# Performance work log

Hardware: AMD Instinct MI355X
Metric: run time of the kernel (lower is better)

## Reference

```python
import math
import jax, jax.numpy as jnp
import numpy as np

B, T, D = 2, 2048, 2048
H = 16
HD = D // H  # 128


def setup_inputs() -> dict:
    key = jax.random.key(0)
    k1, k2, k3 = jax.random.split(key, 3)
    x = jax.random.normal(k1, (B, T, D), dtype=jnp.float32)
    # Linear weights stored as [in, out] for x @ W (torch Linear weight is [out,in])
    w_attn = jax.random.normal(k2, (D, 3 * D), dtype=jnp.float32) * (1.0 / math.sqrt(D))
    w_proj = jax.random.normal(k3, (D, D), dtype=jnp.float32) * (1.0 / math.sqrt(D))
    return {"x": x, "w_attn": w_attn, "w_proj": w_proj}


def reference(x, w_attn, w_proj):
    Bc, Tc, Dc = x.shape
    qkv = x @ w_attn  # [B, T, 3D]
    q, k, v = jnp.split(qkv, 3, axis=2)
    # [B, H, T, HD]
    q = q.reshape(Bc, Tc, H, HD).transpose(0, 2, 1, 3)
    k = k.reshape(Bc, Tc, H, HD).transpose(0, 2, 1, 3)
    v = v.reshape(Bc, Tc, H, HD).transpose(0, 2, 1, 3)
    att = jnp.einsum('bhqd,bhkd->bhqk', q, k) * (1.0 / math.sqrt(HD))
    causal = jnp.tril(jnp.ones((Tc, Tc), dtype=bool))
    att = jnp.where(causal[None, None], att, -jnp.inf)
    att = jax.nn.softmax(att, axis=-1)
    y = jnp.einsum('bhqk,bhkd->bhqd', att, v)
    y = y.transpose(0, 2, 1, 3).reshape(Bc, Tc, Dc)
    return y @ w_proj
```

## Files before the change

kernel.cpp:

```cpp
#include <hip/hip_runtime.h>
#include <hip/hip_bf16.h>

#define B_ 2
#define T_ 2048
#define D_ 2048
#define H_ 16
#define HD_ 128
#define N3_ (3 * D_)
#define M_ (B_ * T_)

typedef __attribute__((ext_vector_type(8))) short short8;
typedef __attribute__((ext_vector_type(4))) short short4v;
typedef __attribute__((ext_vector_type(4))) float floatx4;

__device__ __forceinline__ ushort f2bf(float f) {
  unsigned int x = __float_as_uint(f);
  unsigned int r = (x + 0x7fffu + ((x >> 16) & 1u)) >> 16;
  return (ushort)r;
}

__device__ __forceinline__ void gload_lds16(const ushort* g, ushort* l) {
  __builtin_amdgcn_global_load_lds(
      (const __attribute__((address_space(1))) void*)g,
      (__attribute__((address_space(3))) void*)l, 16, 0, 0);
}

#define CONVB 4096
#define WATB 12288
#define WPTB 4096
__global__ __launch_bounds__(256) void prep(const float* __restrict__ x,
                                            const float* __restrict__ wa,
                                            const float* __restrict__ wp,
                                            ushort* __restrict__ xb,
                                            ushort* __restrict__ wt_attn,
                                            ushort* __restrict__ wt_proj) {
  __shared__ ushort tile[32][33];
  int bid = blockIdx.x;
  if (bid < CONVB) {
    int i = bid * 2048 + threadIdx.x * 8;
    union { ushort u[8]; short8 v; } t;
#pragma unroll
    for (int j = 0; j < 8; j++) t.u[j] = f2bf(x[i + j]);
    *(short8*)(xb + i) = t.v;
    return;
  }
  const float* in;
  ushort* out;
  int N, bx, by;
  if (bid < CONVB + WATB) {
    int id = bid - CONVB;
    N = N3_; bx = id % 192; by = id / 192; in = wa; out = wt_attn;
  } else {
    int id = bid - (CONVB + WATB);
    N = D_; bx = id & 63; by = id >> 6; in = wp; out = wt_proj;
  }
  int n0 = bx * 32, k0 = by * 32;
  int tx = threadIdx.x & 31, ty = threadIdx.x >> 5;
#pragma unroll
  for (int i = ty; i < 32; i += 8)
    tile[i][tx] = f2bf(in[(size_t)(k0 + i) * N + n0 + tx]);
  __syncthreads();
#pragma unroll
  for (int i = ty; i < 32; i += 8)
    out[(size_t)(n0 + i) * 2048 + k0 + tx] = tile[tx][i];
}

__device__ __forceinline__ void gemm128_core(const ushort* __restrict__ Ab,
                                             const ushort* __restrict__ Bb,
                                             ushort* As, ushort* Bs,
                                             floatx4 (&acc)[4][4]) {
  const int K = 2048;
  int tid = threadIdx.x, lane = tid & 63, wave = tid >> 6;
  int l16 = lane & 15, quad = lane >> 4;
  int srow = wave * 16 + (lane >> 2);
  int skq = (lane & 3) * 8;
  const ushort* ag = Ab + (size_t)srow * K + skq;
  const ushort* bg = Bb + (size_t)srow * K + skq;
  ushort* asl = As + wave * 512;
  ushort* bsl = Bs + wave * 512;
  int wr = wave >> 1, wc = wave & 1;
  const int aoff = (wr * 64 + l16) * 32 + quad * 8;
  const int boff = (wc * 64 + l16) * 32 + quad * 8;

  for (int k0 = 0; k0 < K; k0 += 32) {
    __syncthreads();
    gload_lds16(ag + k0, asl);
    gload_lds16(ag + (size_t)64 * K + k0, asl + 2048);
    gload_lds16(bg + k0, bsl);
    gload_lds16(bg + (size_t)64 * K + k0, bsl + 2048);
    __syncthreads();
    short8 af[4], bf[4];
#pragma unroll
    for (int mi = 0; mi < 4; mi++)
      af[mi] = *(const short8*)(As + aoff + mi * 512);
#pragma unroll
    for (int nj = 0; nj < 4; nj++)
      bf[nj] = *(const short8*)(Bs + boff + nj * 512);
#pragma unroll
    for (int mi = 0; mi < 4; mi++)
#pragma unroll
      for (int nj = 0; nj < 4; nj++)
        acc[mi][nj] = __builtin_amdgcn_mfma_f32_16x16x32_bf16(
            af[mi], bf[nj], acc[mi][nj], 0, 0, 0);
  }
}

__global__ __launch_bounds__(256) void gemm_qkv(const ushort* __restrict__ X,
                                                const ushort* __restrict__ Wt,
                                                ushort* __restrict__ qb,
                                                ushort* __restrict__ kb,
                                                ushort* __restrict__ vst) {
  __shared__ ushort As[4096], Bs[4096];
  floatx4 acc[4][4];
#pragma unroll
  for (int i = 0; i < 4; i++)
#pragma unroll
    for (int j = 0; j < 4; j++) acc[i][j] = (floatx4){0.f, 0.f, 0.f, 0.f};

  int m0 = blockIdx.y * 128, n0 = blockIdx.x * 128;
  gemm128_core(X + (size_t)m0 * 2048, Wt + (size_t)n0 * 2048, As, Bs, acc);

  int lane = threadIdx.x & 63, wave = threadIdx.x >> 6;
  int l16 = lane & 15, quad = lane >> 4, wr = wave >> 1, wc = wave & 1;
  int region = n0 >> 11;
  int h = (n0 & 2047) >> 7;
  int b = m0 >> 11, tb = m0 & 2047;
  if (region == 0) {
    ushort* P = qb + ((size_t)(b * H_ + h) * T_ + tb) * HD_;
#pragma unroll
    for (int mi = 0; mi < 4; mi++)
#pragma unroll
      for (int nj = 0; nj < 4; nj++)
#pragma unroll
        for (int r = 0; r < 4; r++)
          P[(size_t)(wr * 64 + mi * 16 + quad * 4 + r) * HD_ + wc * 64 +
            nj * 16 + l16] = f2bf(acc[mi][nj][r]);
  } else if (region == 1) {
    ushort* base = kb + (size_t)(b * H_ + h) * T_ * HD_;
#pragma unroll
    for (int mi = 0; mi < 4; mi++)
#pragma unroll
      for (int nj = 0; nj < 4; nj++) {
        int d = wc * 64 + nj * 16 + l16;
        int dhi = d >> 5, dlo = d & 31;
#pragma unroll
        for (int r = 0; r < 4; r++) {
          int t = tb + wr * 64 + mi * 16 + quad * 4 + r;
          base[(size_t)(t >> 6) * 8192 + dhi * 2048 + (t & 63) * 32 + dlo] =
              f2bf(acc[mi][nj][r]);
        }
      }
  } else {
    ushort* base = vst + (size_t)(b * H_ + h) * T_ * HD_;
#pragma unroll
    for (int mi = 0; mi < 4; mi++)
#pragma unroll
      for (int r = 0; r < 4; r++) {
        int t = tb + wr * 64 + mi * 16 + quad * 4 + r;
        int c = t & 63;
        int p = (c & 15) * 4 + (c >> 4);
        size_t rowbase = (size_t)(t >> 6) * 8192 + (p >> 5) * 4096 + (p & 31);
#pragma unroll
        for (int nj = 0; nj < 4; nj++) {
          int d = wc * 64 + nj * 16 + l16;
          base[rowbase + d * 32] = f2bf(acc[mi][nj][r]);
        }
      }
  }
}

__global__ __launch_bounds__(256) void gemm_proj(const ushort* __restrict__ Y,
                                                 const ushort* __restrict__ Wt,
                                                 float* __restrict__ out) {
  __shared__ ushort As[4096], Bs[4096];
  floatx4 acc[4][4];
#pragma unroll
  for (int i = 0; i < 4; i++)
#pragma unroll
    for (int j = 0; j < 4; j++) acc[i][j] = (floatx4){0.f, 0.f, 0.f, 0.f};

  int m0 = blockIdx.y * 128, n0 = blockIdx.x * 128;
  gemm128_core(Y + (size_t)m0 * 2048, Wt + (size_t)n0 * 2048, As, Bs, acc);

  int lane = threadIdx.x & 63, wave = threadIdx.x >> 6;
  int l16 = lane & 15, quad = lane >> 4, wr = wave >> 1, wc = wave & 1;
#pragma unroll
  for (int mi = 0; mi < 4; mi++)
#pragma unroll
    for (int nj = 0; nj < 4; nj++)
#pragma unroll
      for (int r = 0; r < 4; r++)
        out[(size_t)(m0 + wr * 64 + mi * 16 + quad * 4 + r) * D_ + n0 +
            wc * 64 + nj * 16 + l16] = acc[mi][nj][r];
}

__global__ __launch_bounds__(256) void attn128(const ushort* __restrict__ qb,
                                               const ushort* __restrict__ kst,
                                               const ushort* __restrict__ vst,
                                               ushort* __restrict__ y) {
  __shared__ ushort Ks[8192];
  __shared__ ushort Vs[8192];
  __shared__ ushort Ps[8192];
  int bid = blockIdx.x;
  int bh = bid & 31;
  int qt = (bid < 256) ? (bid >> 5) : (15 - ((bid - 256) >> 5));
  int q0 = qt * 128;
  int tid = threadIdx.x, lane = tid & 63, wave = tid >> 6;
  int l16 = lane & 15, quad = lane >> 4;
  int b = bh >> 4, h = bh & 15;
  const ushort* Q = qb + (size_t)bh * T_ * HD_;
  const ushort* Kt = kst + (size_t)bh * T_ * HD_;
  const ushort* Vt = vst + (size_t)bh * T_ * HD_;
  int qw0 = q0 + wave * 32;

  short8 qf[2][4];
#pragma unroll
  for (int mi = 0; mi < 2; mi++)
#pragma unroll
    for (int kk = 0; kk < 4; kk++)
      qf[mi][kk] = *(const short8*)(Q + (size_t)(qw0 + mi * 16 + l16) * HD_ +
                                    kk * 32 + quad * 8);

  floatx4 o[2][8];
#pragma unroll
  for (int mi = 0; mi < 2; mi++)
#pragma unroll
    for (int nt = 0; nt < 8; nt++) o[mi][nt] = (floatx4){0.f, 0.f, 0.f, 0.f};
  float lrow[2][4];
#pragma unroll
  for (int mi = 0; mi < 2; mi++)
#pragma unroll
    for (int r = 0; r < 4; r++) lrow[mi][r] = 0.f;

  const float scale2 = 0.08838834764831845f * 1.4426950408889634f;
  int ktiles = (q0 >> 6) + 2;

  for (int tile = 0; tile < ktiles; tile++) {
    int kt = tile << 6;
    __syncthreads();
#pragma unroll
    for (int i = 0; i < 4; i++) {
      int g = i * 256 + wave * 64;
      gload_lds16(Kt + (size_t)tile * 8192 + (g + lane) * 8, Ks + g * 8);
      gload_lds16(Vt + (size_t)tile * 8192 + (g + lane) * 8, Vs + g * 8);
    }
    __syncthreads();
    if (kt <= qw0 + 31) {
      floatx4 s[2][4];
#pragma unroll
      for (int mi = 0; mi < 2; mi++)
#pragma unroll
        for (int ng = 0; ng < 4; ng++) s[mi][ng] = (floatx4){0.f, 0.f, 0.f, 0.f};
#pragma unroll
      for (int kk = 0; kk < 4; kk++) {
        short8 kf[4];
#pragma unroll
        for (int ng = 0; ng < 4; ng++)
          kf[ng] = *(const short8*)(Ks + kk * 2048 + (ng * 16 + l16) * 32 +
                                    quad * 8);
#pragma unroll
        for (int mi = 0; mi < 2; mi++)
#pragma unroll
          for (int ng = 0; ng < 4; ng++)
            s[mi][ng] = __builtin_amdgcn_mfma_f32_16x16x32_bf16(
                qf[mi][kk], kf[ng], s[mi][ng], 0, 0, 0);
      }
      if (kt + 63 > qw0) {
#pragma unroll
        for (int mi = 0; mi < 2; mi++)
#pragma unroll
          for (int ng = 0; ng < 4; ng++)
#pragma unroll
            for (int r = 0; r < 4; r++) {
              int key = kt + ng * 16 + l16;
              int qr = qw0 + mi * 16 + quad * 4 + r;
              float p =
                  (key <= qr) ? exp2f(s[mi][ng][r] * scale2) : 0.f;
              s[mi][ng][r] = p;
              lrow[mi][r] += p;
            }
      } else {
#pragma unroll
        for (int mi = 0; mi < 2; mi++)
#pragma unroll
          for (int ng = 0; ng < 4; ng++)
#pragma unroll
            for (int r = 0; r < 4; r++) {
              float p = exp2f(s[mi][ng][r] * scale2);
              s[mi][ng][r] = p;
              lrow[mi][r] += p;
            }
      }
      ushort* Pw = Ps + wave * 2048;
#pragma unroll
      for (int mi = 0; mi < 2; mi++)
#pragma unroll
        for (int r = 0; r < 4; r++) {
          int row = mi * 16 + quad * 4 + r;
          short4v pk;
#pragma unroll
          for (int ng = 0; ng < 4; ng++) pk[ng] = (short)f2bf(s[mi][ng][r]);
          *(short4v*)(Pw + row * 64 + (((l16 >> 1) ^ (row & 7)) << 3) +
                      ((l16 & 1) << 2)) = pk;
        }
      short8 pf[2][2];
#pragma unroll
      for (int mi = 0; mi < 2; mi++)
#pragma unroll
        for (int kc = 0; kc < 2; kc++) {
          int row = mi * 16 + l16;
          pf[mi][kc] = *(const short8*)(
              Pw + row * 64 + ((((kc << 2) + quad) ^ (row & 7)) << 3));
        }
#pragma unroll
      for (int kc = 0; kc < 2; kc++)
#pragma unroll
        for (int nt = 0; nt < 8; nt++) {
          short8 vf = *(const short8*)(Vs + kc * 4096 + (nt * 16 + l16) * 32 +
                                       quad * 8);
#pragma unroll
          for (int mi = 0; mi < 2; mi++)
            o[mi][nt] = __builtin_amdgcn_mfma_f32_16x16x32_bf16(
                pf[mi][kc], vf, o[mi][nt], 0, 0, 0);
        }
    }
  }

#pragma unroll
  for (int off = 1; off < 16; off <<= 1)
#pragma unroll
    for (int mi = 0; mi < 2; mi++)
#pragma unroll
      for (int r = 0; r < 4; r++)
        lrow[mi][r] += __shfl_xor(lrow[mi][r], off);

#pragma unroll
  for (int mi = 0; mi < 2; mi++)
#pragma unroll
    for (int r = 0; r < 4; r++) {
      float inv = 1.f / lrow[mi][r];
      int t = qw0 + mi * 16 + quad * 4 + r;
#pragma unroll
      for (int nt = 0; nt < 8; nt++)
        y[((size_t)(b * T_ + t)) * D_ + h * HD_ + nt * 16 + l16] =
            f2bf(o[mi][nt][r] * inv);
    }
}

extern "C" void kernel_launch(void* const* d_in, const int* in_sizes, int n_in,
                              void* d_out, int out_size, void* d_ws,
                              size_t ws_size, hipStream_t stream) {
  const float* x = (const float*)d_in[0];
  const float* w_attn = (const float*)d_in[1];
  const float* w_proj = (const float*)d_in[2];
  float* out = (float*)d_out;

  char* ws = (char*)d_ws;
  ushort* wt_attn = (ushort*)(ws);
  ushort* wt_proj = (ushort*)(ws + 25165824);
  ushort* qb = (ushort*)(ws + 33554432);
  ushort* kb = (ushort*)(ws + 50331648);
  ushort* vst = (ushort*)(ws + 67108864);
  ushort* xb = (ushort*)(ws + 83886080);
  ushort* yb = xb;
  (void)in_sizes; (void)n_in; (void)out_size; (void)ws_size;

  prep<<<CONVB + WATB + WPTB, 256, 0, stream>>>(x, w_attn, w_proj, xb,
                                                wt_attn, wt_proj);
  gemm_qkv<<<dim3(N3_ / 128, M_ / 128), 256, 0, stream>>>(xb, wt_attn, qb, kb,
                                                          vst);
  attn128<<<B_ * H_ * (T_ / 128), 256, 0, stream>>>(qb, kb, vst, yb);
  gemm_proj<<<dim3(D_ / 128, M_ / 128), 256, 0, stream>>>(yb, wt_proj, out);
}
```

Measured before the change: 407.0 us.

## Pipeline GEMMs with 4-stage LDS ring and 256x128 tiles on 512 threads

```diff
diff --git a/kernel.cpp b/kernel.cpp
--- a/kernel.cpp
+++ b/kernel.cpp
@@ -65,62 +65,132 @@
     out[(size_t)(n0 + i) * 2048 + k0 + tx] = tile[tx][i];
 }
 
-__device__ __forceinline__ void gemm128_core(const ushort* __restrict__ Ab,
-                                             const ushort* __restrict__ Bb,
-                                             ushort* As, ushort* Bs,
-                                             floatx4 (&acc)[4][4]) {
-  const int K = 2048;
+#define GBM 256
+#define GBN 128
+#define GBK 32
+#define GKD 2048
+#define GNT (GKD / GBK)
+#define A_US (GBM * GBK)
+#define B_US (GBN * GBK)
+#define BUF_US (A_US + B_US)
+
+struct GPtr {
+  const ushort* a0;
+  const ushort* a1;
+  const ushort* b0;
+};
+
+template <bool STG, int VM>
+__device__ __forceinline__ void ktile(const GPtr& gp, size_t kpos,
+                                      const ushort* Ac, const ushort* Bc,
+                                      ushort* As_s, ushort* Bs_s, int w512,
+                                      const int (&arow)[4], const int (&brow)[4],
+                                      floatx4 (&acc)[4][4]) {
+  short8 af[4], bf[4];
+#pragma unroll
+  for (int mi = 0; mi < 4; mi++)
+    af[mi] = *(const short8*)(Ac + arow[mi]);
+#pragma unroll
+  for (int nj = 0; nj < 4; nj++)
+    bf[nj] = *(const short8*)(Bc + brow[nj]);
+  if constexpr (STG) {
+    gload_lds16(gp.a0 + kpos, As_s + w512);
+    gload_lds16(gp.a1 + kpos, As_s + 4096 + w512);
+    gload_lds16(gp.b0 + kpos, Bs_s + w512);
+  }
+  __builtin_amdgcn_s_barrier();
+  asm volatile("s_waitcnt lgkmcnt(0)" ::: "memory");
+  __builtin_amdgcn_sched_barrier(0);
+  __builtin_amdgcn_s_setprio(1);
+#pragma unroll
+  for (int mi = 0; mi < 4; mi++)
+#pragma unroll
+    for (int nj = 0; nj < 4; nj++)
+      acc[mi][nj] = __builtin_amdgcn_mfma_f32_16x16x32_bf16(
+          af[mi], bf[nj], acc[mi][nj], 0, 0, 0);
+  __builtin_amdgcn_s_setprio(0);
+  if constexpr (VM == 6) {
+    asm volatile("s_waitcnt vmcnt(6)" ::: "memory");
+    __builtin_amdgcn_sched_barrier(0);
+  } else if constexpr (VM == 3) {
+    asm volatile("s_waitcnt vmcnt(3)" ::: "memory");
+    __builtin_amdgcn_sched_barrier(0);
+  } else if constexpr (VM == 0) {
+    asm volatile("s_waitcnt vmcnt(0)" ::: "memory");
+    __builtin_amdgcn_sched_barrier(0);
+  }
+  __builtin_amdgcn_s_barrier();
+}
+
+__device__ __forceinline__ void gemm_core(const ushort* __restrict__ Ag,
+                                          const ushort* __restrict__ Bg,
+                                          ushort* lds, floatx4 (&acc)[4][4]) {
+  int tid = threadIdx.x;
+  int lane = tid & 63, wave = tid >> 6;
+  int l16 = lane & 15, quad = lane >> 4;
+  int wr = wave >> 1, wc = wave & 1;
+  int w512 = wave * 512;
+
+  GPtr gp;
+  gp.a0 = Ag + (size_t)(tid >> 2) * GKD + (tid & 3) * 8;
+  gp.a1 = gp.a0 + (size_t)128 * GKD;
+  gp.b0 = Bg + (size_t)(tid >> 2) * GKD + (tid & 3) * 8;
+
+  int arow[4], brow[4];
+#pragma unroll
+  for (int i = 0; i < 4; i++) {
+    arow[i] = (wr * 64 + i * 16 + l16) * GBK + quad * 8;
+    brow[i] = (wc * 64 + i * 16 + l16) * GBK + quad * 8;
+  }
+
+#pragma unroll
+  for (int t = 0; t < 3; t++) {
+    ushort* As_s = lds + t * BUF_US;
+    gload_lds16(gp.a0 + (size_t)t * GBK, As_s + w512);
+    gload_lds16(gp.a1 + (size_t)t * GBK, As_s + 4096 + w512);
+    gload_lds16(gp.b0 + (size_t)t * GBK, As_s + A_US + w512);
+  }
+  asm volatile("s_waitcnt vmcnt(6)" ::: "memory");
+  __builtin_amdgcn_sched_barrier(0);
+  __builtin_amdgcn_s_barrier();
+
+  int ci = 0, si = 3;
+#pragma unroll 1
+  for (int t = 0; t < GNT - 3; ++t) {
+    const ushort* bc = lds + ci * BUF_US;
+    ushort* bs = lds + si * BUF_US;
+    ktile<true, 6>(gp, (size_t)(t + 3) * GBK, bc, bc + A_US, bs, bs + A_US,
+                   w512, arow, brow, acc);
+    ci = (ci + 1) & 3;
+    si = (si + 1) & 3;
+  }
+  const ushort* bc = lds + ci * BUF_US;
+  ci = (ci + 1) & 3;
+  ktile<false, 3>(gp, 0, bc, bc + A_US, lds, lds + A_US, w512, arow, brow, acc);
+  bc = lds + ci * BUF_US;
+  ci = (ci + 1) & 3;
+  ktile<false, 0>(gp, 0, bc, bc + A_US, lds, lds + A_US, w512, arow, brow, acc);
+  bc = lds + ci * BUF_US;
+  ktile<false, -1>(gp, 0, bc, bc + A_US, lds, lds + A_US, w512, arow, brow,
+                   acc);
+}
+
+__global__ __launch_bounds__(512, 2) void gemm_qkv(const ushort* __restrict__ X,
+                                                   const ushort* __restrict__ Wt,
+                                                   ushort* __restrict__ qb,
+                                                   ushort* __restrict__ kb,
+                                                   ushort* __restrict__ vst) {
+  __shared__ __align__(16) ushort lds[4 * BUF_US];
+  floatx4 acc[4][4];
+#pragma unroll
+  for (int i = 0; i < 4; i++)
+#pragma unroll
+    for (int j = 0; j < 4; j++) acc[i][j] = (floatx4){0.f, 0.f, 0.f, 0.f};
+
+  int m0 = blockIdx.y * GBM, n0 = blockIdx.x * GBN;
+  gemm_core(X + (size_t)m0 * GKD, Wt + (size_t)n0 * GKD, lds, acc);
+
   int tid = threadIdx.x, lane = tid & 63, wave = tid >> 6;
-  int l16 = lane & 15, quad = lane >> 4;
-  int srow = wave * 16 + (lane >> 2);
-  int skq = (lane & 3) * 8;
-  const ushort* ag = Ab + (size_t)srow * K + skq;
-  const ushort* bg = Bb + (size_t)srow * K + skq;
-  ushort* asl = As + wave * 512;
-  ushort* bsl = Bs + wave * 512;
-  int wr = wave >> 1, wc = wave & 1;
-  const int aoff = (wr * 64 + l16) * 32 + quad * 8;
-  const int boff = (wc * 64 + l16) * 32 + quad * 8;
-
-  for (int k0 = 0; k0 < K; k0 += 32) {
-    __syncthreads();
-    gload_lds16(ag + k0, asl);
-    gload_lds16(ag + (size_t)64 * K + k0, asl + 2048);
-    gload_lds16(bg + k0, bsl);
-    gload_lds16(bg + (size_t)64 * K + k0, bsl + 2048);
-    __syncthreads();
-    short8 af[4], bf[4];
-#pragma unroll
-    for (int mi = 0; mi < 4; mi++)
-      af[mi] = *(const short8*)(As + aoff + mi * 512);
-#pragma unroll
-    for (int nj = 0; nj < 4; nj++)
-      bf[nj] = *(const short8*)(Bs + boff + nj * 512);
-#pragma unroll
-    for (int mi = 0; mi < 4; mi++)
-#pragma unroll
-      for (int nj = 0; nj < 4; nj++)
-        acc[mi][nj] = __builtin_amdgcn_mfma_f32_16x16x32_bf16(
-            af[mi], bf[nj], acc[mi][nj], 0, 0, 0);
-  }
-}
-
-__global__ __launch_bounds__(256) void gemm_qkv(const ushort* __restrict__ X,
-                                                const ushort* __restrict__ Wt,
-                                                ushort* __restrict__ qb,
-                                                ushort* __restrict__ kb,
-                                                ushort* __restrict__ vst) {
-  __shared__ ushort As[4096], Bs[4096];
-  floatx4 acc[4][4];
-#pragma unroll
-  for (int i = 0; i < 4; i++)
-#pragma unroll
-    for (int j = 0; j < 4; j++) acc[i][j] = (floatx4){0.f, 0.f, 0.f, 0.f};
-
-  int m0 = blockIdx.y * 128, n0 = blockIdx.x * 128;
-  gemm128_core(X + (size_t)m0 * 2048, Wt + (size_t)n0 * 2048, As, Bs, acc);
-
-  int lane = threadIdx.x & 63, wave = threadIdx.x >> 6;
   int l16 = lane & 15, quad = lane >> 4, wr = wave >> 1, wc = wave & 1;
   int region = n0 >> 11;
   int h = (n0 & 2047) >> 7;
@@ -169,20 +239,20 @@
   }
 }
 
-__global__ __launch_bounds__(256) void gemm_proj(const ushort* __restrict__ Y,
-                                                 const ushort* __restrict__ Wt,
-                                                 float* __restrict__ out) {
-  __shared__ ushort As[4096], Bs[4096];
+__global__ __launch_bounds__(512, 2) void gemm_proj(const ushort* __restrict__ Y,
+                                                    const ushort* __restrict__ Wt,
+                                                    float* __restrict__ out) {
+  __shared__ __align__(16) ushort lds[4 * BUF_US];
   floatx4 acc[4][4];
 #pragma unroll
   for (int i = 0; i < 4; i++)
 #pragma unroll
     for (int j = 0; j < 4; j++) acc[i][j] = (floatx4){0.f, 0.f, 0.f, 0.f};
 
-  int m0 = blockIdx.y * 128, n0 = blockIdx.x * 128;
-  gemm128_core(Y + (size_t)m0 * 2048, Wt + (size_t)n0 * 2048, As, Bs, acc);
-
-  int lane = threadIdx.x & 63, wave = threadIdx.x >> 6;
+  int m0 = blockIdx.y * GBM, n0 = blockIdx.x * GBN;
+  gemm_core(Y + (size_t)m0 * GKD, Wt + (size_t)n0 * GKD, lds, acc);
+
+  int tid = threadIdx.x, lane = tid & 63, wave = tid >> 6;
   int l16 = lane & 15, quad = lane >> 4, wr = wave >> 1, wc = wave & 1;
 #pragma unroll
   for (int mi = 0; mi < 4; mi++)
@@ -367,8 +437,8 @@
 
   prep<<<CONVB + WATB + WPTB, 256, 0, stream>>>(x, w_attn, w_proj, xb,
                                                 wt_attn, wt_proj);
-  gemm_qkv<<<dim3(N3_ / 128, M_ / 128), 256, 0, stream>>>(xb, wt_attn, qb, kb,
+  gemm_qkv<<<dim3(N3_ / GBN, M_ / GBM), 512, 0, stream>>>(xb, wt_attn, qb, kb,
                                                           vst);
   attn128<<<B_ * H_ * (T_ / 128), 256, 0, stream>>>(qb, kb, vst, yb);
-  gemm_proj<<<dim3(D_ / 128, M_ / 128), 256, 0, stream>>>(yb, wt_proj, out);
-}
+  gemm_proj<<<dim3(D_ / GBN, M_ / GBM), 512, 0, stream>>>(yb, wt_proj, out);
+}
```

After: 375.4 us. -7.7%, faster.
